# Performance work log

Measured on AMD Instinct MI355X. Metric: run time of the kernel, lower is better.

Reference implementation:

```python
import jax, jax.numpy as jnp
import numpy as np

N = 50000       # nodes
E = 1250000     # edges
DIM = 64
H = 16
DPH = DIM // H  # 4
LN_EPS = 1e-5


def setup_inputs() -> dict:
    key = jax.random.key(0)
    ks = jax.random.split(key, 10)
    return {
        "node_feat": jax.random.normal(ks[0], (N, DIM), jnp.float32),
        "edge_feat": jax.random.normal(ks[1], (E, H, DPH), jnp.float32),
        "node_vec": jax.random.normal(ks[2], (N, 3, DIM), jnp.float32),
        "radial": jax.random.uniform(ks[3], (E,), jnp.float32),
        "ln_g": jnp.ones((DIM,), jnp.float32),
        "ln_b": jnp.zeros((DIM,), jnp.float32),
        "qkv_w": jax.random.normal(ks[4], (DIM, 3 * DIM), jnp.float32) / np.sqrt(DIM).astype(np.float32),
        "qkv_b": jnp.zeros((3 * DIM,), jnp.float32),
        "vec_w": jax.random.normal(ks[5], (DIM, 2 * DIM), jnp.float32) / np.sqrt(DIM).astype(np.float32),
        "out_w": jax.random.normal(ks[6], (DIM, 2 * DIM), jnp.float32) / np.sqrt(DIM).astype(np.float32),
        "out_b": jnp.zeros((2 * DIM,), jnp.float32),
        "row": jax.random.randint(ks[7], (E,), 0, N, jnp.int32),
        "col": jax.random.randint(ks[8], (E,), 0, N, jnp.int32),
        "natoms": N,
    }


def reference(node_feat, edge_feat, node_vec, radial, ln_g, ln_b,
              qkv_w, qkv_b, vec_w, out_w, out_b, row, col, natoms):
    # LayerNorm (biased variance, as torch)
    mu = jnp.mean(node_feat, axis=-1, keepdims=True)
    var = jnp.mean(jnp.square(node_feat - mu), axis=-1, keepdims=True)
    x = (node_feat - mu) * jax.lax.rsqrt(var + LN_EPS) * ln_g + ln_b

    # QKV projection -> [N, H, 3*DPH], split
    qkv = (x @ qkv_w + qkv_b).reshape(-1, H, 3 * DPH)
    q = qkv[..., :DPH]
    k = qkv[..., DPH:2 * DPH]
    v = qkv[..., 2 * DPH:]

    # Gather by edge indices, gated dot-product attention per edge  [E, H]
    attn = jax.nn.gelu(jnp.sum(q[row] * k[col], axis=-1), approximate=False) * radial[:, None]

    # Equivariant vector gate  [N, DIM]
    iv = node_vec @ vec_w  # [N, 3, 2*DIM]
    input_dot = jnp.sum(iv[..., :DIM] * iv[..., DIM:], axis=-2)

    # Edge messages and scatter-add into nodes
    m = v[col] * edge_feat * attn[..., None]          # [E, H, DPH]
    m_agg = jax.ops.segment_sum(m, row, num_segments=natoms)  # [N, H, DPH]
    m_agg = m_agg.reshape(natoms, DIM)

    out = m_agg @ out_w + out_b                        # [N, 2*DIM]
    return input_dot * out[..., :DIM] + out[..., DIM:]
```

## Files before the change

### kernel.cpp

```cpp
#include <hip/hip_runtime.h>
#include <math.h>

#define DIM 64
#define NW 4
#define NPB 4
#define CAP 64

__device__ __forceinline__ float waveReduceSum(float v) {
    #pragma unroll
    for (int off = 1; off < 64; off <<= 1)
        v += __shfl_xor(v, off, 64);
    return v;
}

__global__ __launch_bounds__(256) void qkv_kernel(
    const float* __restrict__ node_feat,
    const float* __restrict__ ln_g, const float* __restrict__ ln_b,
    const float* __restrict__ qkv_w, const float* __restrict__ qkv_b,
    float* __restrict__ q, float* __restrict__ k, float* __restrict__ v,
    int* __restrict__ deg, int* __restrict__ ovcnt,
    int N)
{
    __shared__ float  wlds[64 * 192];
    __shared__ float4 xs[NW][NPB][16];
    const int wave = threadIdx.x >> 6, lane = threadIdx.x & 63;

    for (int i = blockIdx.x * 256 + threadIdx.x; i < N; i += gridDim.x * 256)
        deg[i] = 0;
    if (blockIdx.x == 0 && threadIdx.x == 0) *ovcnt = 0;

    for (int idx = threadIdx.x; idx < 64 * 192; idx += 256) {
        int d = idx / 192, j = idx - d * 192;
        int jj = j & 63, sec = j >> 6;
        int c = 12 * (jj >> 2) + (jj & 3) + 4 * sec;
        wlds[idx] = qkv_w[d * 192 + c];
    }
    const int c0 = 12 * (lane >> 2) + (lane & 3);
    const float b0 = qkv_b[c0], b1 = qkv_b[c0 + 4], b2 = qkv_b[c0 + 8];
    const float gg = ln_g[lane], bb = ln_b[lane];
    __syncthreads();

    const int nstride = gridDim.x * NW * NPB;
    for (int n0 = (blockIdx.x * NW + wave) * NPB; n0 < N; n0 += nstride) {
        const int cnt = min(NPB, N - n0);
        float acc0[NPB], acc1[NPB], acc2[NPB];
        #pragma unroll
        for (int i = 0; i < NPB; ++i) {
            acc0[i] = b0; acc1[i] = b1; acc2[i] = b2;
            if (i < cnt) {
                float nf = node_feat[(size_t)(n0 + i) * DIM + lane];
                float mu = waveReduceSum(nf) * (1.0f / 64.0f);
                float dv = nf - mu;
                float var = waveReduceSum(dv * dv) * (1.0f / 64.0f);
                float x = dv * rsqrtf(var + 1e-5f) * gg + bb;
                ((float*)&xs[wave][i][0])[lane] = x;
            }
        }
        #pragma unroll 4
        for (int d4 = 0; d4 < 16; ++d4) {
            float4 xv[NPB];
            #pragma unroll
            for (int i = 0; i < NPB; ++i) xv[i] = xs[wave][i][d4];
            #pragma unroll
            for (int u = 0; u < 4; ++u) {
                int d = d4 * 4 + u;
                float w0 = wlds[d * 192 + lane];
                float w1 = wlds[d * 192 + lane + 64];
                float w2 = wlds[d * 192 + lane + 128];
                #pragma unroll
                for (int i = 0; i < NPB; ++i) {
                    float xd = (&xv[i].x)[u];
                    acc0[i] = fmaf(xd, w0, acc0[i]);
                    acc1[i] = fmaf(xd, w1, acc1[i]);
                    acc2[i] = fmaf(xd, w2, acc2[i]);
                }
            }
        }
        #pragma unroll
        for (int i = 0; i < NPB; ++i) if (i < cnt) {
            size_t off = (size_t)(n0 + i) * DIM + lane;
            q[off] = acc0[i]; k[off] = acc1[i]; v[off] = acc2[i];
        }
    }
}

__global__ __launch_bounds__(256) void vec_kernel(
    const float* __restrict__ node_vec,
    const float* __restrict__ vec_w,
    float* __restrict__ input_dot,
    const int* __restrict__ row,
    const int* __restrict__ col,
    int* __restrict__ deg,
    int2* __restrict__ perm2,
    int* __restrict__ ovcnt,
    int* __restrict__ ovlist,
    int N, int E)
{
    __shared__ float  vlds[64 * 128];
    __shared__ float4 nvs[NW][NPB][3][16];
    const int wave = threadIdx.x >> 6, lane = threadIdx.x & 63;

    for (int idx = threadIdx.x; idx < 64 * 128; idx += 256)
        vlds[idx] = vec_w[idx];
    __syncthreads();

    const int nstride = gridDim.x * NW * NPB;
    for (int n0 = (blockIdx.x * NW + wave) * NPB; n0 < N; n0 += nstride) {
        const int cnt = min(NPB, N - n0);
        float a0[NPB][3], a1[NPB][3];
        #pragma unroll
        for (int i = 0; i < NPB; ++i) {
            #pragma unroll
            for (int s = 0; s < 3; ++s) {
                a0[i][s] = 0.f; a1[i][s] = 0.f;
                if (i < cnt)
                    ((float*)&nvs[wave][i][s][0])[lane] =
                        node_vec[((size_t)(n0 + i) * 3 + s) * DIM + lane];
            }
        }
        #pragma unroll 2
        for (int d4 = 0; d4 < 16; ++d4) {
            #pragma unroll
            for (int u = 0; u < 4; ++u) {
                int d = d4 * 4 + u;
                float w0 = vlds[d * 128 + lane];
                float w1 = vlds[d * 128 + lane + 64];
                #pragma unroll
                for (int i = 0; i < NPB; ++i) {
                    #pragma unroll
                    for (int s = 0; s < 3; ++s) {
                        float nv = ((float*)&nvs[wave][i][s][d4])[u];
                        a0[i][s] = fmaf(nv, w0, a0[i][s]);
                        a1[i][s] = fmaf(nv, w1, a1[i][s]);
                    }
                }
            }
        }
        #pragma unroll
        for (int i = 0; i < NPB; ++i) if (i < cnt) {
            size_t off = (size_t)(n0 + i) * DIM + lane;
            input_dot[off] = a0[i][0] * a1[i][0] + a0[i][1] * a1[i][1]
                           + a0[i][2] * a1[i][2];
        }
    }

    for (int e = blockIdx.x * 256 + threadIdx.x; e < E; e += gridDim.x * 256) {
        int r = row[e];
        int slot = atomicAdd(&deg[r], 1);
        if (slot < CAP) {
            perm2[(size_t)r * CAP + slot] = make_int2(e, col[e]);
        } else {
            int o = atomicAdd(ovcnt, 1);
            ovlist[o] = e;
        }
    }
}

__global__ __launch_bounds__(256) void agg_kernel(
    const float* __restrict__ q,
    const float* __restrict__ k,
    const float* __restrict__ v,
    const float* __restrict__ edge_feat,
    const float* __restrict__ radial,
    const int2* __restrict__ perm2,
    const int* __restrict__ deg,
    float* __restrict__ m_agg,
    int N)
{
    const int wave = threadIdx.x >> 6, lane = threadIdx.x & 63;
    for (int n = blockIdx.x * NW + wave; n < N; n += gridDim.x * NW) {
        const int cn = min(deg[n], CAP);
        const int2* pr = perm2 + (size_t)n * CAP;
        int2 myec = make_int2(0, 0);
        float myrad = 0.0f;
        if (lane < cn) {
            myec = pr[lane];
            myrad = radial[myec.x];
        }
        const float qd = q[(size_t)n * DIM + lane];
        float acc = 0.0f;
        #pragma unroll 4
        for (int j = 0; j < cn; ++j) {
            int   e   = __shfl(myec.x, j, 64);
            int   c   = __shfl(myec.y, j, 64);
            float rad = __shfl(myrad, j, 64);
            float kd = k[(size_t)c * DIM + lane];
            float vd = v[(size_t)c * DIM + lane];
            float ef = __builtin_nontemporal_load(&edge_feat[(size_t)e * DIM + lane]);
            float p = qd * kd;
            p += __shfl_xor(p, 1, 64);
            p += __shfl_xor(p, 2, 64);
            float g = 0.5f * p * (1.0f + erff(p * 0.70710678118654752f));
            acc = fmaf(vd * ef, g * rad, acc);
        }
        m_agg[(size_t)n * DIM + lane] = acc;
    }
}

__global__ __launch_bounds__(256) void ovf_kernel(
    const float* __restrict__ q,
    const float* __restrict__ k,
    const float* __restrict__ v,
    const float* __restrict__ edge_feat,
    const float* __restrict__ radial,
    const int* __restrict__ row,
    const int* __restrict__ col,
    const int* __restrict__ ovcnt,
    const int* __restrict__ ovlist,
    float* __restrict__ m_agg)
{
    const int wave = threadIdx.x >> 6, lane = threadIdx.x & 63;
    const int ovn = *ovcnt;
    for (int i = blockIdx.x * NW + wave; i < ovn; i += gridDim.x * NW) {
        int e = ovlist[i];
        int r = row[e], c = col[e];
        float p = q[(size_t)r * DIM + lane] * k[(size_t)c * DIM + lane];
        p += __shfl_xor(p, 1, 64);
        p += __shfl_xor(p, 2, 64);
        float g = 0.5f * p * (1.0f + erff(p * 0.70710678118654752f));
        float a = g * radial[e];
        float m = v[(size_t)c * DIM + lane] * edge_feat[(size_t)e * DIM + lane] * a;
        atomicAdd(&m_agg[(size_t)r * DIM + lane], m);
    }
}

__global__ __launch_bounds__(256) void out_kernel(
    const float* __restrict__ m_agg,
    const float* __restrict__ input_dot,
    const float* __restrict__ out_w,
    const float* __restrict__ out_b,
    float* __restrict__ result,
    int N)
{
    __shared__ float  olds[64 * 128];
    __shared__ float4 ms[NW][NPB][16];
    const int wave = threadIdx.x >> 6, lane = threadIdx.x & 63;

    for (int idx = threadIdx.x; idx < 64 * 128; idx += 256)
        olds[idx] = out_w[idx];
    const float ob0 = out_b[lane], ob1 = out_b[lane + 64];
    __syncthreads();

    const int nstride = gridDim.x * NW * NPB;
    for (int n0 = (blockIdx.x * NW + wave) * NPB; n0 < N; n0 += nstride) {
        const int cnt = min(NPB, N - n0);
        float o0[NPB], o1[NPB];
        #pragma unroll
        for (int i = 0; i < NPB; ++i) {
            o0[i] = ob0; o1[i] = ob1;
            if (i < cnt)
                ((float*)&ms[wave][i][0])[lane] =
                    m_agg[(size_t)(n0 + i) * DIM + lane];
        }
        #pragma unroll 4
        for (int d4 = 0; d4 < 16; ++d4) {
            float4 mv[NPB];
            #pragma unroll
            for (int i = 0; i < NPB; ++i) mv[i] = ms[wave][i][d4];
            #pragma unroll
            for (int u = 0; u < 4; ++u) {
                int d = d4 * 4 + u;
                float w0 = olds[d * 128 + lane];
                float w1 = olds[d * 128 + lane + 64];
                #pragma unroll
                for (int i = 0; i < NPB; ++i) {
                    float md = (&mv[i].x)[u];
                    o0[i] = fmaf(md, w0, o0[i]);
                    o1[i] = fmaf(md, w1, o1[i]);
                }
            }
        }
        #pragma unroll
        for (int i = 0; i < NPB; ++i) if (i < cnt) {
            size_t off = (size_t)(n0 + i) * DIM + lane;
            result[off] = input_dot[off] * o0[i] + o1[i];
        }
    }
}

extern "C" void kernel_launch(void* const* d_in, const int* in_sizes, int n_in,
                              void* d_out, int out_size, void* d_ws, size_t ws_size,
                              hipStream_t stream)
{
    const float* node_feat = (const float*)d_in[0];
    const float* edge_feat = (const float*)d_in[1];
    const float* node_vec  = (const float*)d_in[2];
    const float* radial    = (const float*)d_in[3];
    const float* ln_g      = (const float*)d_in[4];
    const float* ln_b      = (const float*)d_in[5];
    const float* qkv_w     = (const float*)d_in[6];
    const float* qkv_b     = (const float*)d_in[7];
    const float* vec_w     = (const float*)d_in[8];
    const float* out_w     = (const float*)d_in[9];
    const float* out_b     = (const float*)d_in[10];
    const int*   row       = (const int*)d_in[11];
    const int*   col       = (const int*)d_in[12];

    const int N = in_sizes[0] / DIM;
    const int E = in_sizes[3];

    float* ws    = (float*)d_ws;
    float* q     = ws;
    float* k     = q    + (size_t)N * DIM;
    float* v     = k    + (size_t)N * DIM;
    float* idot  = v    + (size_t)N * DIM;
    float* m_agg = idot + (size_t)N * DIM;
    int2*  perm2  = (int2*)(m_agg + (size_t)N * DIM);
    int*   deg    = (int*)(perm2 + (size_t)N * CAP);
    int*   ovcnt  = deg + N;
    int*   ovlist = ovcnt + 1;

    const int grid_nodes = 768;
    const int grid_agg   = (N + NW - 1) / NW;

    qkv_kernel<<<grid_nodes, 256, 0, stream>>>(node_feat, ln_g, ln_b,
                                               qkv_w, qkv_b, q, k, v,
                                               deg, ovcnt, N);
    vec_kernel<<<grid_nodes, 256, 0, stream>>>(node_vec, vec_w, idot,
                                               row, col, deg, perm2,
                                               ovcnt, ovlist, N, E);
    agg_kernel<<<grid_agg, 256, 0, stream>>>(q, k, v, edge_feat, radial,
                                             perm2, deg, m_agg, N);
    ovf_kernel<<<256, 256, 0, stream>>>(q, k, v, edge_feat, radial,
                                        row, col, ovcnt, ovlist, m_agg);
    out_kernel<<<grid_nodes, 256, 0, stream>>>(m_agg, idot, out_w, out_b,
                                               (float*)d_out, N);
}
```

Before: 734.1 us.

## Fuse aggregation with output projection and software-pipeline neighbor gathers

Merges the per-node edge aggregation and the output linear layer into one kernel, so m_agg no longer makes a global round trip and one launch disappears. Overflow edges are now scattered first into a zeroed m_agg, and the fused kernel adds that buffer only for high-degree nodes. The edge loop keeps a depth-4 register queue of k/v/edge_feat loads so gathers overlap with compute. The out_w matrix is now read from global/L1 per node instead of staged in LDS, which may cost some bandwidth, and the deg/ovcnt clearing moves to memset calls.

```diff
diff --git a/kernel.cpp b/kernel.cpp
--- a/kernel.cpp
+++ b/kernel.cpp
@@ -5,6 +5,7 @@
 #define NW 4
 #define NPB 4
 #define CAP 64
+#define PIPE 4
 
 __device__ __forceinline__ float waveReduceSum(float v) {
     #pragma unroll
@@ -18,16 +19,11 @@
     const float* __restrict__ ln_g, const float* __restrict__ ln_b,
     const float* __restrict__ qkv_w, const float* __restrict__ qkv_b,
     float* __restrict__ q, float* __restrict__ k, float* __restrict__ v,
-    int* __restrict__ deg, int* __restrict__ ovcnt,
     int N)
 {
     __shared__ float  wlds[64 * 192];
     __shared__ float4 xs[NW][NPB][16];
     const int wave = threadIdx.x >> 6, lane = threadIdx.x & 63;
-
-    for (int i = blockIdx.x * 256 + threadIdx.x; i < N; i += gridDim.x * 256)
-        deg[i] = 0;
-    if (blockIdx.x == 0 && threadIdx.x == 0) *ovcnt = 0;
 
     for (int idx = threadIdx.x; idx < 64 * 192; idx += 256) {
         int d = idx / 192, j = idx - d * 192;
@@ -156,47 +152,6 @@
     }
 }
 
-__global__ __launch_bounds__(256) void agg_kernel(
-    const float* __restrict__ q,
-    const float* __restrict__ k,
-    const float* __restrict__ v,
-    const float* __restrict__ edge_feat,
-    const float* __restrict__ radial,
-    const int2* __restrict__ perm2,
-    const int* __restrict__ deg,
-    float* __restrict__ m_agg,
-    int N)
-{
-    const int wave = threadIdx.x >> 6, lane = threadIdx.x & 63;
-    for (int n = blockIdx.x * NW + wave; n < N; n += gridDim.x * NW) {
-        const int cn = min(deg[n], CAP);
-        const int2* pr = perm2 + (size_t)n * CAP;
-        int2 myec = make_int2(0, 0);
-        float myrad = 0.0f;
-        if (lane < cn) {
-            myec = pr[lane];
-            myrad = radial[myec.x];
-        }
-        const float qd = q[(size_t)n * DIM + lane];
-        float acc = 0.0f;
-        #pragma unroll 4
-        for (int j = 0; j < cn; ++j) {
-            int   e   = __shfl(myec.x, j, 64);
-            int   c   = __shfl(myec.y, j, 64);
-            float rad = __shfl(myrad, j, 64);
-            float kd = k[(size_t)c * DIM + lane];
-            float vd = v[(size_t)c * DIM + lane];
-            float ef = __builtin_nontemporal_load(&edge_feat[(size_t)e * DIM + lane]);
-            float p = qd * kd;
-            p += __shfl_xor(p, 1, 64);
-            p += __shfl_xor(p, 2, 64);
-            float g = 0.5f * p * (1.0f + erff(p * 0.70710678118654752f));
-            acc = fmaf(vd * ef, g * rad, acc);
-        }
-        m_agg[(size_t)n * DIM + lane] = acc;
-    }
-}
-
 __global__ __launch_bounds__(256) void ovf_kernel(
     const float* __restrict__ q,
     const float* __restrict__ k,
@@ -224,7 +179,14 @@
     }
 }
 
-__global__ __launch_bounds__(256) void out_kernel(
+__global__ __launch_bounds__(256) void agg_kernel(
+    const float* __restrict__ q,
+    const float* __restrict__ kptr,
+    const float* __restrict__ vptr,
+    const float* __restrict__ edge_feat,
+    const float* __restrict__ radial,
+    const int2* __restrict__ perm2,
+    const int* __restrict__ deg,
     const float* __restrict__ m_agg,
     const float* __restrict__ input_dot,
     const float* __restrict__ out_w,
@@ -232,50 +194,69 @@
     float* __restrict__ result,
     int N)
 {
-    __shared__ float  olds[64 * 128];
-    __shared__ float4 ms[NW][NPB][16];
+    __shared__ float accs[NW][64];
     const int wave = threadIdx.x >> 6, lane = threadIdx.x & 63;
-
-    for (int idx = threadIdx.x; idx < 64 * 128; idx += 256)
-        olds[idx] = out_w[idx];
     const float ob0 = out_b[lane], ob1 = out_b[lane + 64];
-    __syncthreads();
-
-    const int nstride = gridDim.x * NW * NPB;
-    for (int n0 = (blockIdx.x * NW + wave) * NPB; n0 < N; n0 += nstride) {
-        const int cnt = min(NPB, N - n0);
-        float o0[NPB], o1[NPB];
-        #pragma unroll
-        for (int i = 0; i < NPB; ++i) {
-            o0[i] = ob0; o1[i] = ob1;
-            if (i < cnt)
-                ((float*)&ms[wave][i][0])[lane] =
-                    m_agg[(size_t)(n0 + i) * DIM + lane];
-        }
-        #pragma unroll 4
-        for (int d4 = 0; d4 < 16; ++d4) {
-            float4 mv[NPB];
-            #pragma unroll
-            for (int i = 0; i < NPB; ++i) mv[i] = ms[wave][i][d4];
-            #pragma unroll
-            for (int u = 0; u < 4; ++u) {
-                int d = d4 * 4 + u;
-                float w0 = olds[d * 128 + lane];
-                float w1 = olds[d * 128 + lane + 64];
-                #pragma unroll
-                for (int i = 0; i < NPB; ++i) {
-                    float md = (&mv[i].x)[u];
-                    o0[i] = fmaf(md, w0, o0[i]);
-                    o1[i] = fmaf(md, w1, o1[i]);
+
+#define ISSUE(J, S) do {                                                   \
+        if ((J) < cn) {                                                    \
+            int e_ = __shfl(myec.x, (J), 64);                              \
+            int c_ = __shfl(myec.y, (J), 64);                              \
+            kq[S] = kptr[(c_ << 6) + lane];                                \
+            vq[S] = vptr[(c_ << 6) + lane];                                \
+            eq[S] = __builtin_nontemporal_load(                            \
+                        &edge_feat[((size_t)(unsigned)e_ << 6) + lane]);   \
+        }                                                                  \
+    } while (0)
+
+    for (int n = blockIdx.x * NW + wave; n < N; n += gridDim.x * NW) {
+        const int draw = deg[n];
+        const int cn = min(draw, CAP);
+        int2 myec = make_int2(0, 0);
+        float myrad = 0.0f;
+        if (lane < cn) {
+            myec = perm2[(size_t)n * CAP + lane];
+            myrad = radial[myec.x];
+        }
+        const float qd = q[(n << 6) + lane];
+        float idv = input_dot[(n << 6) + lane];
+
+        float kq[PIPE], vq[PIPE], eq[PIPE];
+        #pragma unroll
+        for (int s = 0; s < PIPE; ++s) ISSUE(s, s);
+
+        float acc = 0.0f;
+        for (int j0 = 0; j0 < cn; j0 += PIPE) {
+            #pragma unroll
+            for (int s = 0; s < PIPE; ++s) {
+                const int j = j0 + s;
+                if (j < cn) {
+                    float kd = kq[s], vd = vq[s], ef = eq[s];
+                    ISSUE(j + PIPE, s);
+                    float rad = __shfl(myrad, j, 64);
+                    float p = qd * kd;
+                    p += __shfl_xor(p, 1, 64);
+                    p += __shfl_xor(p, 2, 64);
+                    float g = 0.5f * p *
+                              (1.0f + erff(p * 0.70710678118654752f));
+                    acc = fmaf(vd * ef, g * rad, acc);
                 }
             }
         }
-        #pragma unroll
-        for (int i = 0; i < NPB; ++i) if (i < cnt) {
-            size_t off = (size_t)(n0 + i) * DIM + lane;
-            result[off] = input_dot[off] * o0[i] + o1[i];
-        }
-    }
+
+        if (draw > CAP) acc += m_agg[(n << 6) + lane];
+
+        accs[wave][lane] = acc;
+        float o0 = ob0, o1 = ob1;
+        #pragma unroll 8
+        for (int d = 0; d < 64; ++d) {
+            float md = accs[wave][d];
+            o0 = fmaf(md, out_w[d * 128 + lane], o0);
+            o1 = fmaf(md, out_w[d * 128 + 64 + lane], o1);
+        }
+        result[(n << 6) + lane] = idv * o0 + o1;
+    }
+#undef ISSUE
 }
 
 extern "C" void kernel_launch(void* const* d_in, const int* in_sizes, int n_in,
@@ -305,24 +286,25 @@
     float* v     = k    + (size_t)N * DIM;
     float* idot  = v    + (size_t)N * DIM;
     float* m_agg = idot + (size_t)N * DIM;
-    int2*  perm2  = (int2*)(m_agg + (size_t)N * DIM);
-    int*   deg    = (int*)(perm2 + (size_t)N * CAP);
-    int*   ovcnt  = deg + N;
-    int*   ovlist = ovcnt + 1;
+    int2*  perm2 = (int2*)(m_agg + (size_t)N * DIM);
+    int*   deg   = (int*)(perm2 + (size_t)N * CAP);
+    int*   ovcnt = deg + N;
+    int*   ovlist= ovcnt + 1;
 
     const int grid_nodes = 768;
     const int grid_agg   = (N + NW - 1) / NW;
 
+    hipMemsetAsync(m_agg, 0, (size_t)N * DIM * sizeof(float), stream);
+    hipMemsetAsync(deg,   0, (size_t)(N + 1) * sizeof(int), stream);
+
     qkv_kernel<<<grid_nodes, 256, 0, stream>>>(node_feat, ln_g, ln_b,
-                                               qkv_w, qkv_b, q, k, v,
-                                               deg, ovcnt, N);
+                                               qkv_w, qkv_b, q, k, v, N);
     vec_kernel<<<grid_nodes, 256, 0, stream>>>(node_vec, vec_w, idot,
                                                row, col, deg, perm2,
                                                ovcnt, ovlist, N, E);
-    agg_kernel<<<grid_agg, 256, 0, stream>>>(q, k, v, edge_feat, radial,
-                                             perm2, deg, m_agg, N);
     ovf_kernel<<<256, 256, 0, stream>>>(q, k, v, edge_feat, radial,
                                         row, col, ovcnt, ovlist, m_agg);
-    out_kernel<<<grid_nodes, 256, 0, stream>>>(m_agg, idot, out_w, out_b,
-                                               (float*)d_out, N);
-}
+    agg_kernel<<<grid_agg, 256, 0, stream>>>(q, k, v, edge_feat, radial,
+                                             perm2, deg, m_agg, idot,
+                                             out_w, out_b, (float*)d_out, N);
+}
```

After: 762.5 us. 1.04x slower.
